# Kernel optimization log

Measured on AMD Instinct MI355X. Metric: run time of the kernel, lower is better.

The kernel has to match this reference:

```python
import jax, jax.numpy as jnp
import numpy as np

N_LAYERS = 5
HID = 64
N_FF = 512
N_VOCAB = 500
N_NODES = 50000
N_EDGES = 800000


def setup_inputs() -> dict:
    key = jax.random.key(0)
    ks = jax.random.split(key, 12)
    x = jax.random.randint(ks[0], (N_NODES,), 0, N_VOCAB)
    edge_index = jax.random.randint(ks[1], (2, N_EDGES), 0, N_NODES)
    edge_attr = jax.random.normal(ks[2], (N_EDGES, 4), dtype=jnp.float32)
    s = 1.0 / float(np.sqrt(HID))
    vert_emb = jax.random.normal(ks[3], (N_VOCAB + 1, HID), dtype=jnp.float32) * s
    vert_emb = vert_emb.at[N_VOCAB].set(0.0)  # padding_idx row
    edge_emb_w = jax.random.normal(ks[4], (4, HID), dtype=jnp.float32) * 0.5
    edge_lin_w = jax.random.normal(ks[5], (N_LAYERS, HID, HID), dtype=jnp.float32) * s
    rel_w = jax.random.normal(ks[6], (N_LAYERS, HID, HID), dtype=jnp.float32) * s
    rel_b = jnp.zeros((N_LAYERS, HID), dtype=jnp.float32)
    root_w = jax.random.normal(ks[7], (N_LAYERS, HID, HID), dtype=jnp.float32) * s
    res_w = jax.random.normal(ks[8], (N_LAYERS, HID, HID), dtype=jnp.float32) * s
    head_w1 = jax.random.normal(ks[9], (HID, N_FF), dtype=jnp.float32) * s
    head_b1 = jnp.zeros((N_FF,), dtype=jnp.float32)
    head_w2 = jax.random.normal(ks[10], (N_FF, 1), dtype=jnp.float32) * (1.0 / float(np.sqrt(N_FF)))
    head_b2 = jnp.zeros((1,), dtype=jnp.float32)
    return dict(x=x, edge_index=edge_index, edge_attr=edge_attr, vert_emb=vert_emb,
                edge_emb_w=edge_emb_w, edge_lin_w=edge_lin_w, rel_w=rel_w, rel_b=rel_b,
                root_w=root_w, res_w=res_w, head_w1=head_w1, head_b1=head_b1,
                head_w2=head_w2, head_b2=head_b2)


def reference(x, edge_index, edge_attr, vert_emb, edge_emb_w, edge_lin_w, rel_w, rel_b,
              root_w, res_w, head_w1, head_b1, head_w2, head_b2):
    src, dst = edge_index[0], edge_index[1]
    h = vert_emb[x]                         # [N, HID] embedding lookup
    ea = edge_attr @ edge_emb_w             # [E, HID] edge embedding
    n = h.shape[0]
    for l in range(N_LAYERS):
        ea_l = ea @ edge_lin_w[l]           # ResGraphModule.edge_lin
        # GraphConv(aggr='add'): lin_rel(scatter_add(x_src * e)) + lin_root(x)
        msg = h[src] * ea_l                 # [E, HID] gather + modulate
        agg = jax.ops.segment_sum(msg, dst, num_segments=n)
        out = agg @ rel_w[l] + rel_b[l] + h @ root_w[l]
        out = jax.nn.relu(out)
        h = out + h @ res_w[l]              # residual branch (res_lin)
    # head MLP (dropout is identity in eval mode); torch GELU is exact erf GELU
    hft = jax.nn.gelu(h @ head_w1 + head_b1, approximate=False)
    return hft @ head_w2 + head_b2          # [N, 1]
```

## Files before the change

kernel.cpp:

```cpp
#include <hip/hip_runtime.h>
#include <math.h>

#define HID 64
#define NLAY 5
#define NFF 512

typedef __attribute__((ext_vector_type(8))) short bf16x8;
typedef __attribute__((ext_vector_type(4))) float f32x4;

__device__ __forceinline__ unsigned short f2bf(float x) {
  unsigned int b = __float_as_uint(x);
  b += 0x7FFFu + ((b >> 16) & 1u);
  return (unsigned short)(b >> 16);
}
__device__ __forceinline__ float bf2f(unsigned short u) {
  return __uint_as_float((unsigned int)u << 16);
}

__global__ void prep_all_kernel(const float* __restrict__ edge_emb_w,
                                const float* __restrict__ edge_lin_w,
                                const float* __restrict__ w1,
                                const float* __restrict__ rel_w,
                                const float* __restrict__ root_w,
                                const float* __restrict__ res_w,
                                float* __restrict__ Wl,
                                unsigned short* __restrict__ w1bhi,
                                unsigned short* __restrict__ w1blo,
                                unsigned short* __restrict__ nwhi,
                                unsigned short* __restrict__ nwlo) {
  int bid = blockIdx.x;
  int tid = threadIdx.x;
  if (bid < 5) {
    int j = tid >> 6;
    int d = tid & 63;
    const float* ew = edge_emb_w + j * HID;
    const float* lw = edge_lin_w + bid * HID * HID;
    float acc = 0.f;
#pragma unroll
    for (int k = 0; k < HID; ++k) acc = fmaf(ew[k], lw[k * HID + d], acc);
    Wl[(bid * 4 + j) * HID + d] = acc;
  } else if (bid < 21) {
    int t = (bid - 5) * 256 + tid;
    int f = t >> 6;
    int l = t & 63;
    int kt = f >> 5;
    int nt = f & 31;
    int krow = kt * 32 + (l >> 4) * 8;
    int col = nt * 16 + (l & 15);
#pragma unroll
    for (int j = 0; j < 8; ++j) {
      float v = w1[(size_t)(krow + j) * NFF + col];
      unsigned short hi = f2bf(v);
      unsigned short lo = f2bf(v - bf2f(hi));
      w1bhi[(size_t)t * 8 + j] = hi;
      w1blo[(size_t)t * 8 + j] = lo;
    }
  } else {
    int mi = bid - 21;
    int layer = mi / 3, mat = mi % 3;
    const float* W = (mat == 0 ? rel_w : (mat == 1 ? root_w : res_w)) +
                     (size_t)layer * HID * HID;
#pragma unroll
    for (int half = 0; half < 2; ++half) {
      int t = half * 256 + tid;
      int f = t >> 6, l = t & 63;
      int kt = f >> 2, nt = f & 3;
      int krow = kt * 32 + (l >> 4) * 8;
      int col = nt * 16 + (l & 15);
#pragma unroll
      for (int j = 0; j < 8; ++j) {
        float v = W[(size_t)(krow + j) * HID + col];
        unsigned short hi = f2bf(v);
        unsigned short lo = f2bf(v - bf2f(hi));
        size_t off = (((size_t)mi * 8 + f) * 64 + l) * 8 + j;
        nwhi[off] = hi;
        nwlo[off] = lo;
      }
    }
  }
}

__global__ void embed_kernel(const int* __restrict__ x,
                             const float* __restrict__ vert_emb,
                             float* __restrict__ h,
                             unsigned short* __restrict__ h16,
                             int* __restrict__ deg, int n) {
  int idx = blockIdx.x * blockDim.x + threadIdx.x;
  if (idx >= n * HID) return;
  int node = idx >> 6;
  int d = idx & 63;
  float v = vert_emb[x[node] * HID + d];
  h[idx] = v;
  h16[idx] = f2bf(v);
  if (d == 0) deg[node] = 0;
}


__global__ void hist_kernel(const int* __restrict__ dst, int* __restrict__ deg, int E) {
  int e = blockIdx.x * blockDim.x + threadIdx.x;
  if (e < E) atomicAdd(&deg[dst[e]], 1);
}

__global__ void bsum_kernel(const int* __restrict__ deg, int* __restrict__ bsum, int n) {
  __shared__ int s[256];
  int t = threadIdx.x;
  int i = blockIdx.x * 256 + t;
  s[t] = (i < n) ? deg[i] : 0;
  __syncthreads();
#pragma unroll
  for (int off = 128; off > 0; off >>= 1) {
    if (t < off) s[t] += s[t + off];
    __syncthreads();
  }
  if (t == 0) bsum[blockIdx.x] = s[0];
}

__global__ void bscan_kernel(const int* __restrict__ bsum, int* __restrict__ boff, int nb) {
  __shared__ int s[256];
  int t = threadIdx.x;
  int v = (t < nb) ? bsum[t] : 0;
  s[t] = v;
  __syncthreads();
#pragma unroll
  for (int off = 1; off < 256; off <<= 1) {
    int u = (t >= off) ? s[t - off] : 0;
    __syncthreads();
    s[t] += u;
    __syncthreads();
  }
  if (t < nb) boff[t] = s[t] - v;
}

__global__ void scan3_kernel(const int* __restrict__ deg, const int* __restrict__ boff,
                             int* __restrict__ row_ptr, int* __restrict__ cursor, int n) {
  __shared__ int s[256];
  int t = threadIdx.x;
  int i = blockIdx.x * 256 + t;
  int v = (i < n) ? deg[i] : 0;
  s[t] = v;
  __syncthreads();
#pragma unroll
  for (int off = 1; off < 256; off <<= 1) {
    int u = (t >= off) ? s[t - off] : 0;
    __syncthreads();
    s[t] += u;
    __syncthreads();
  }
  if (i < n) {
    int excl = boff[blockIdx.x] + s[t] - v;
    row_ptr[i] = excl;
    cursor[i] = excl;
    if (i == n - 1) row_ptr[n] = excl + v;
  }
}

__global__ void scatter_kernel(const int* __restrict__ src,
                               const int* __restrict__ dst,
                               const float4* __restrict__ edge_attr,
                               int* __restrict__ cursor,
                               float4* __restrict__ csr2, int E) {
  int e = blockIdx.x * blockDim.x + threadIdx.x;
  if (e >= E) return;
  int pos = atomicAdd(&cursor[dst[e]], 1);
  csr2[(size_t)2 * pos] = edge_attr[e];
  float4 m;
  m.x = __int_as_float(src[e]);
  m.y = 0.f; m.z = 0.f; m.w = 0.f;
  csr2[(size_t)2 * pos + 1] = m;
}

__global__ __launch_bounds__(256, 4)
void layer_fused_kernel(const int* __restrict__ row_ptr,
                        const float4* __restrict__ csr2,
                        const float* __restrict__ Wl,
                        const float* __restrict__ h,
                        const unsigned short* __restrict__ h16,
                        const unsigned short* __restrict__ nwhi,
                        const unsigned short* __restrict__ nwlo,
                        const float* __restrict__ rel_b,
                        float* __restrict__ hn,
                        unsigned short* __restrict__ hn16, int n) {
  __shared__ float sagg[16][65];
  int tid = threadIdx.x;
  int w = tid >> 6;
  int d = tid & 63;
  int base = blockIdx.x * 16;
  float w0 = Wl[d], w1_ = Wl[HID + d], w2_ = Wl[2 * HID + d], w3_ = Wl[3 * HID + d];
  const int* csri = (const int*)csr2;
  for (int i = 0; i < 4; ++i) {
    int node = base + w * 4 + i;
    float P0 = 0.f, P1 = 0.f, P2 = 0.f, P3 = 0.f;
    if (node < n) {
      int beg = __builtin_amdgcn_readfirstlane(row_ptr[node]);
      int end = __builtin_amdgcn_readfirstlane(row_ptr[node + 1]);
      int j = beg;
      for (; j + 16 <= end; j += 16) {
        int ss[16];
        float hh[16];
        float4 ee[16];
#pragma unroll
        for (int u = 0; u < 16; ++u) ss[u] = csri[((size_t)2 * (j + u) + 1) * 4];
#pragma unroll
        for (int u = 0; u < 16; ++u) hh[u] = bf2f(h16[(size_t)ss[u] * HID + d]);
#pragma unroll
        for (int u = 0; u < 16; ++u) ee[u] = csr2[(size_t)2 * (j + u)];
#pragma unroll
        for (int u = 0; u < 16; ++u) {
          P0 = fmaf(ee[u].x, hh[u], P0);
          P1 = fmaf(ee[u].y, hh[u], P1);
          P2 = fmaf(ee[u].z, hh[u], P2);
          P3 = fmaf(ee[u].w, hh[u], P3);
        }
      }
      for (; j + 4 <= end; j += 4) {
        int ss[4];
        float hh[4];
        float4 ee[4];
#pragma unroll
        for (int u = 0; u < 4; ++u) ss[u] = csri[((size_t)2 * (j + u) + 1) * 4];
#pragma unroll
        for (int u = 0; u < 4; ++u) hh[u] = bf2f(h16[(size_t)ss[u] * HID + d]);
#pragma unroll
        for (int u = 0; u < 4; ++u) ee[u] = csr2[(size_t)2 * (j + u)];
#pragma unroll
        for (int u = 0; u < 4; ++u) {
          P0 = fmaf(ee[u].x, hh[u], P0);
          P1 = fmaf(ee[u].y, hh[u], P1);
          P2 = fmaf(ee[u].z, hh[u], P2);
          P3 = fmaf(ee[u].w, hh[u], P3);
        }
      }
      for (; j < end; ++j) {
        int s0 = csri[((size_t)2 * j + 1) * 4];
        float4 e0 = csr2[(size_t)2 * j];
        float h0 = bf2f(h16[(size_t)s0 * HID + d]);
        P0 = fmaf(e0.x, h0, P0);
        P1 = fmaf(e0.y, h0, P1);
        P2 = fmaf(e0.z, h0, P2);
        P3 = fmaf(e0.w, h0, P3);
      }
    }
    float acc = fmaf(P3, w3_, fmaf(P2, w2_, fmaf(P1, w1_, P0 * w0)));
    sagg[w * 4 + i][d] = acc;
  }
  __syncthreads();
  int l = tid & 63;
  int q = l & 15;
  int g = l >> 4;
  int node = base + q;
  if (node >= n) node = n - 1;
  bf16x8 aghi[2], aglo[2], ahhi[2], ahlo[2];
#pragma unroll
  for (int kt = 0; kt < 2; ++kt) {
    int koff = kt * 32 + g * 8;
    const float* hp = h + (size_t)node * HID + koff;
    ahhi[kt] = *(const bf16x8*)(h16 + (size_t)node * HID + koff);
#pragma unroll
    for (int j = 0; j < 8; ++j) {
      float av = sagg[q][koff + j];
      unsigned short hi = f2bf(av);
      aghi[kt][j] = (short)hi;
      aglo[kt][j] = (short)f2bf(av - bf2f(hi));
      float r = hp[j] - bf2f((unsigned short)ahhi[kt][j]);
      ahlo[kt][j] = (short)f2bf(r);
    }
  }
  f32x4 aR = {0.f, 0.f, 0.f, 0.f};
  f32x4 aO = {0.f, 0.f, 0.f, 0.f};
  f32x4 aS = {0.f, 0.f, 0.f, 0.f};
#pragma unroll
  for (int kt = 0; kt < 2; ++kt) {
    int f = kt * 4 + w;
    const bf16x8* bRh = (const bf16x8*)(nwhi + (((size_t)0 * 8 + f) * 64 + l) * 8);
    const bf16x8* bRl = (const bf16x8*)(nwlo + (((size_t)0 * 8 + f) * 64 + l) * 8);
    const bf16x8* bOh = (const bf16x8*)(nwhi + (((size_t)1 * 8 + f) * 64 + l) * 8);
    const bf16x8* bOl = (const bf16x8*)(nwlo + (((size_t)1 * 8 + f) * 64 + l) * 8);
    const bf16x8* bSh = (const bf16x8*)(nwhi + (((size_t)2 * 8 + f) * 64 + l) * 8);
    const bf16x8* bSl = (const bf16x8*)(nwlo + (((size_t)2 * 8 + f) * 64 + l) * 8);
    aR = __builtin_amdgcn_mfma_f32_16x16x32_bf16(aglo[kt], *bRh, aR, 0, 0, 0);
    aR = __builtin_amdgcn_mfma_f32_16x16x32_bf16(aghi[kt], *bRl, aR, 0, 0, 0);
    aR = __builtin_amdgcn_mfma_f32_16x16x32_bf16(aghi[kt], *bRh, aR, 0, 0, 0);
    aO = __builtin_amdgcn_mfma_f32_16x16x32_bf16(ahlo[kt], *bOh, aO, 0, 0, 0);
    aO = __builtin_amdgcn_mfma_f32_16x16x32_bf16(ahhi[kt], *bOl, aO, 0, 0, 0);
    aO = __builtin_amdgcn_mfma_f32_16x16x32_bf16(ahhi[kt], *bOh, aO, 0, 0, 0);
    aS = __builtin_amdgcn_mfma_f32_16x16x32_bf16(ahlo[kt], *bSh, aS, 0, 0, 0);
    aS = __builtin_amdgcn_mfma_f32_16x16x32_bf16(ahhi[kt], *bSl, aS, 0, 0, 0);
    aS = __builtin_amdgcn_mfma_f32_16x16x32_bf16(ahhi[kt], *bSh, aS, 0, 0, 0);
  }
  int col = w * 16 + q;
  float bd = rel_b[col];
#pragma unroll
  for (int r = 0; r < 4; ++r) {
    int nd = base + g * 4 + r;
    if (nd < n) {
      float v = fmaxf(aR[r] + aO[r] + bd, 0.f) + aS[r];
      hn[(size_t)nd * HID + col] = v;
      hn16[(size_t)nd * HID + col] = f2bf(v);
    }
  }
}

__global__ __launch_bounds__(256, 4)
void head_kernel(const float* __restrict__ h,
                 const unsigned short* __restrict__ h16,
                 const unsigned short* __restrict__ w1bhi,
                 const unsigned short* __restrict__ w1blo,
                 const float* __restrict__ b1,
                 const float* __restrict__ w2,
                 const float* __restrict__ b2,
                 float* __restrict__ out, int n) {
  __shared__ float red[4][16];
  int tid = threadIdx.x;
  int w = tid >> 6;
  int l = tid & 63;
  int row = l & 15;
  int g = l >> 4;
  int base = blockIdx.x * 16;
  int node = base + row;
  if (node >= n) node = n - 1;
  f32x4 acc[8];
#pragma unroll
  for (int t = 0; t < 8; ++t) acc[t] = (f32x4){0.f, 0.f, 0.f, 0.f};
#pragma unroll
  for (int kt = 0; kt < 2; ++kt) {
    int koff = kt * 32 + g * 8;
    bf16x8 ahi = *(const bf16x8*)(h16 + (size_t)node * HID + koff);
    const float* hp = h + (size_t)node * HID + koff;
    bf16x8 alo;
#pragma unroll
    for (int j = 0; j < 8; ++j) {
      float r = hp[j] - bf2f((unsigned short)ahi[j]);
      alo[j] = (short)f2bf(r);
    }
#pragma unroll
    for (int t = 0; t < 8; ++t) {
      int f = kt * 32 + w * 8 + t;
      bf16x8 bhi = *(const bf16x8*)(w1bhi + (size_t)f * 512 + l * 8);
      bf16x8 blo = *(const bf16x8*)(w1blo + (size_t)f * 512 + l * 8);
      acc[t] = __builtin_amdgcn_mfma_f32_16x16x32_bf16(alo, bhi, acc[t], 0, 0, 0);
      acc[t] = __builtin_amdgcn_mfma_f32_16x16x32_bf16(ahi, blo, acc[t], 0, 0, 0);
      acc[t] = __builtin_amdgcn_mfma_f32_16x16x32_bf16(ahi, bhi, acc[t], 0, 0, 0);
    }
  }
  float s0 = 0.f, s1 = 0.f, s2 = 0.f, s3 = 0.f;
#pragma unroll
  for (int t = 0; t < 8; ++t) {
    int ff = (w * 8 + t) * 16 + row;
    float bb = b1[ff];
    float ww = w2[ff];
    float xv, gl;
    xv = acc[t][0] + bb; gl = 0.5f * xv * (1.f + erff(xv * 0.70710678118654752f)); s0 = fmaf(gl, ww, s0);
    xv = acc[t][1] + bb; gl = 0.5f * xv * (1.f + erff(xv * 0.70710678118654752f)); s1 = fmaf(gl, ww, s1);
    xv = acc[t][2] + bb; gl = 0.5f * xv * (1.f + erff(xv * 0.70710678118654752f)); s2 = fmaf(gl, ww, s2);
    xv = acc[t][3] + bb; gl = 0.5f * xv * (1.f + erff(xv * 0.70710678118654752f)); s3 = fmaf(gl, ww, s3);
  }
#pragma unroll
  for (int off = 1; off < 16; off <<= 1) {
    s0 += __shfl_xor(s0, off);
    s1 += __shfl_xor(s1, off);
    s2 += __shfl_xor(s2, off);
    s3 += __shfl_xor(s3, off);
  }
  if ((l & 15) == 0) {
    red[w][g * 4 + 0] = s0;
    red[w][g * 4 + 1] = s1;
    red[w][g * 4 + 2] = s2;
    red[w][g * 4 + 3] = s3;
  }
  __syncthreads();
  if (tid < 16 && base + tid < n)
    out[base + tid] = red[0][tid] + red[1][tid] + red[2][tid] + red[3][tid] + b2[0];
}

extern "C" void kernel_launch(void* const* d_in, const int* in_sizes, int n_in,
                              void* d_out, int out_size, void* d_ws, size_t ws_size,
                              hipStream_t stream) {
  const int*   x          = (const int*)d_in[0];
  const int*   edge_index = (const int*)d_in[1];
  const float* edge_attr  = (const float*)d_in[2];
  const float* vert_emb   = (const float*)d_in[3];
  const float* edge_emb_w = (const float*)d_in[4];
  const float* edge_lin_w = (const float*)d_in[5];
  const float* rel_w      = (const float*)d_in[6];
  const float* rel_b      = (const float*)d_in[7];
  const float* root_w     = (const float*)d_in[8];
  const float* res_w      = (const float*)d_in[9];
  const float* w1         = (const float*)d_in[10];
  const float* b1         = (const float*)d_in[11];
  const float* w2         = (const float*)d_in[12];
  const float* b2         = (const float*)d_in[13];

  const int n = in_sizes[0];
  const int E = in_sizes[2] / 4;
  const int* src = edge_index;
  const int* dst = edge_index + E;
  const int nb = (n + 255) / 256;

  float* ws   = (float*)d_ws;
  float* Wl   = ws;
  float* hA   = ws + 2048;
  float* hB   = hA + (size_t)n * HID;
  float4* csr2 = (float4*)(hB + (size_t)n * HID);
  int* row_ptr = (int*)(csr2 + (size_t)2 * E);
  int* cursor  = row_ptr + (n + 1);
  int* deg     = cursor + n;
  int* bsum    = deg + n;
  int* boff    = bsum + 256;
  unsigned short* w1bhi = (unsigned short*)(((size_t)(boff + 256) + 15) & ~(size_t)15);
  unsigned short* w1blo = w1bhi + 64 * 512;
  unsigned short* nwhi  = w1blo + 64 * 512;
  unsigned short* nwlo  = nwhi + NLAY * 3 * 4096;
  unsigned short* h16A  = nwlo + NLAY * 3 * 4096;
  unsigned short* h16B  = h16A + (size_t)n * HID;

  prep_all_kernel<<<dim3(36), dim3(256), 0, stream>>>(
      edge_emb_w, edge_lin_w, w1, rel_w, root_w, res_w,
      Wl, w1bhi, w1blo, nwhi, nwlo);

  int totalHD = n * HID;
  embed_kernel<<<dim3((totalHD + 255) / 256), dim3(256), 0, stream>>>(
      x, vert_emb, hA, h16A, deg, n);

  hist_kernel<<<dim3((E + 255) / 256), dim3(256), 0, stream>>>(dst, deg, E);
  bsum_kernel<<<dim3(nb), dim3(256), 0, stream>>>(deg, bsum, n);
  bscan_kernel<<<dim3(1), dim3(256), 0, stream>>>(bsum, boff, nb);
  scan3_kernel<<<dim3(nb), dim3(256), 0, stream>>>(deg, boff, row_ptr, cursor, n);
  scatter_kernel<<<dim3((E + 255) / 256), dim3(256), 0, stream>>>(
      src, dst, (const float4*)edge_attr, cursor, csr2, E);

  float* hc = hA;
  float* hx = hB;
  unsigned short* h16c = h16A;
  unsigned short* h16x = h16B;
  for (int l = 0; l < NLAY; ++l) {
    layer_fused_kernel<<<dim3((n + 15) / 16), dim3(256), 0, stream>>>(
        row_ptr, csr2, Wl + l * 4 * HID, hc, h16c,
        nwhi + (size_t)l * 3 * 4096, nwlo + (size_t)l * 3 * 4096,
        rel_b + l * HID, hx, h16x, n);
    float* t = hc; hc = hx; hx = t;
    unsigned short* t16 = h16c; h16c = h16x; h16x = t16;
  }

  head_kernel<<<dim3((n + 15) / 16), dim3(256), 0, stream>>>(
      hc, h16c, w1bhi, w1blo, b1, w2, b2, (float*)d_out, n);
}
```

Measured before the change: 451.3 us.

## Split layer into gather and MFMA kernels with lane-broadcast src and double-buffered loads

Each fused layer kernel is split into a gather kernel, with one wave per node, and a separate MFMA node-transform kernel that reads the aggregate from a global buffer. The gather loads up to 64 source indices with one coalesced load per wave and broadcasts them with readlane. It then double-buffers chunks of 8 edge loads so the next chunk is in flight while the current one is accumulated. This aims to raise memory-level parallelism and reduce per-edge index load latency. In exchange it adds a global round trip for the aggregate (n×64 floats written and read per layer) and a second kernel launch per layer.

```diff
diff --git a/kernel.cpp b/kernel.cpp
--- a/kernel.cpp
+++ b/kernel.cpp
@@ -169,95 +169,102 @@
   csr2[(size_t)2 * pos + 1] = m;
 }
 
+#define GLOAD_CHUNK(HH, EE, c)                                            \
+  {                                                                       \
+    int cbase = 8 * (c);                                                  \
+    _Pragma("unroll")                                                     \
+    for (int u = 0; u < 8; ++u) {                                         \
+      int idx = cbase + u;                                                \
+      int cl = (idx < bcnt) ? idx : 0;                                    \
+      int su = __builtin_amdgcn_readlane(srcv, cl);                       \
+      HH[u] = bf2f(h16[(size_t)su * HID + d]);                            \
+      float4 ev = csr2[(size_t)2 * (blk + cl)];                           \
+      if (idx >= bcnt) { ev.x = 0.f; ev.y = 0.f; ev.z = 0.f; ev.w = 0.f; } \
+      EE[u] = ev;                                                         \
+    }                                                                     \
+  }
+
+#define GCONSUME_CHUNK(HH, EE)                                            \
+  {                                                                       \
+    _Pragma("unroll")                                                     \
+    for (int u = 0; u < 8; ++u) {                                         \
+      P0 = fmaf(EE[u].x, HH[u], P0);                                      \
+      P1 = fmaf(EE[u].y, HH[u], P1);                                      \
+      P2 = fmaf(EE[u].z, HH[u], P2);                                      \
+      P3 = fmaf(EE[u].w, HH[u], P3);                                      \
+    }                                                                     \
+  }
+
 __global__ __launch_bounds__(256, 4)
-void layer_fused_kernel(const int* __restrict__ row_ptr,
-                        const float4* __restrict__ csr2,
-                        const float* __restrict__ Wl,
-                        const float* __restrict__ h,
-                        const unsigned short* __restrict__ h16,
-                        const unsigned short* __restrict__ nwhi,
-                        const unsigned short* __restrict__ nwlo,
-                        const float* __restrict__ rel_b,
-                        float* __restrict__ hn,
-                        unsigned short* __restrict__ hn16, int n) {
-  __shared__ float sagg[16][65];
+void gather_kernel(const int* __restrict__ row_ptr,
+                   const float4* __restrict__ csr2,
+                   const float* __restrict__ Wl,
+                   const unsigned short* __restrict__ h16,
+                   float* __restrict__ agg, int n) {
+  int wid = threadIdx.x >> 6;
+  int d = threadIdx.x & 63;
+  int node = blockIdx.x * 4 + wid;
+  if (node >= n) return;
+  int beg = __builtin_amdgcn_readfirstlane(row_ptr[node]);
+  int end = __builtin_amdgcn_readfirstlane(row_ptr[node + 1]);
+  const int* csri = (const int*)csr2;
+  float P0 = 0.f, P1 = 0.f, P2 = 0.f, P3 = 0.f;
+  for (int blk = beg; blk < end; blk += 64) {
+    int bcnt = end - blk;
+    if (bcnt > 64) bcnt = 64;
+    int li = (d < bcnt) ? d : bcnt - 1;
+    int srcv = csri[((size_t)2 * (blk + li) + 1) * 4];
+    int nch = (bcnt + 7) >> 3;
+    float hhA[8], hhB[8];
+    float4 eeA[8], eeB[8];
+    GLOAD_CHUNK(hhA, eeA, 0)
+    int c = 0;
+    while (c < nch) {
+      if (c + 1 < nch) {
+        GLOAD_CHUNK(hhB, eeB, c + 1)
+        GCONSUME_CHUNK(hhA, eeA)
+        ++c;
+        if (c + 1 < nch) { GLOAD_CHUNK(hhA, eeA, c + 1) }
+        GCONSUME_CHUNK(hhB, eeB)
+        ++c;
+      } else {
+        GCONSUME_CHUNK(hhA, eeA)
+        ++c;
+      }
+    }
+  }
+  float w0 = Wl[d], w1_ = Wl[HID + d], w2_ = Wl[2 * HID + d], w3_ = Wl[3 * HID + d];
+  float acc = fmaf(P3, w3_, fmaf(P2, w2_, fmaf(P1, w1_, P0 * w0)));
+  agg[(size_t)node * HID + d] = acc;
+}
+
+__global__ __launch_bounds__(256, 4)
+void node_mfma_kernel(const float* __restrict__ h,
+                      const unsigned short* __restrict__ h16,
+                      const float* __restrict__ agg,
+                      const unsigned short* __restrict__ nwhi,
+                      const unsigned short* __restrict__ nwlo,
+                      const float* __restrict__ rel_b,
+                      float* __restrict__ hn,
+                      unsigned short* __restrict__ hn16, int n) {
   int tid = threadIdx.x;
   int w = tid >> 6;
-  int d = tid & 63;
-  int base = blockIdx.x * 16;
-  float w0 = Wl[d], w1_ = Wl[HID + d], w2_ = Wl[2 * HID + d], w3_ = Wl[3 * HID + d];
-  const int* csri = (const int*)csr2;
-  for (int i = 0; i < 4; ++i) {
-    int node = base + w * 4 + i;
-    float P0 = 0.f, P1 = 0.f, P2 = 0.f, P3 = 0.f;
-    if (node < n) {
-      int beg = __builtin_amdgcn_readfirstlane(row_ptr[node]);
-      int end = __builtin_amdgcn_readfirstlane(row_ptr[node + 1]);
-      int j = beg;
-      for (; j + 16 <= end; j += 16) {
-        int ss[16];
-        float hh[16];
-        float4 ee[16];
-#pragma unroll
-        for (int u = 0; u < 16; ++u) ss[u] = csri[((size_t)2 * (j + u) + 1) * 4];
-#pragma unroll
-        for (int u = 0; u < 16; ++u) hh[u] = bf2f(h16[(size_t)ss[u] * HID + d]);
-#pragma unroll
-        for (int u = 0; u < 16; ++u) ee[u] = csr2[(size_t)2 * (j + u)];
-#pragma unroll
-        for (int u = 0; u < 16; ++u) {
-          P0 = fmaf(ee[u].x, hh[u], P0);
-          P1 = fmaf(ee[u].y, hh[u], P1);
-          P2 = fmaf(ee[u].z, hh[u], P2);
-          P3 = fmaf(ee[u].w, hh[u], P3);
-        }
-      }
-      for (; j + 4 <= end; j += 4) {
-        int ss[4];
-        float hh[4];
-        float4 ee[4];
-#pragma unroll
-        for (int u = 0; u < 4; ++u) ss[u] = csri[((size_t)2 * (j + u) + 1) * 4];
-#pragma unroll
-        for (int u = 0; u < 4; ++u) hh[u] = bf2f(h16[(size_t)ss[u] * HID + d]);
-#pragma unroll
-        for (int u = 0; u < 4; ++u) ee[u] = csr2[(size_t)2 * (j + u)];
-#pragma unroll
-        for (int u = 0; u < 4; ++u) {
-          P0 = fmaf(ee[u].x, hh[u], P0);
-          P1 = fmaf(ee[u].y, hh[u], P1);
-          P2 = fmaf(ee[u].z, hh[u], P2);
-          P3 = fmaf(ee[u].w, hh[u], P3);
-        }
-      }
-      for (; j < end; ++j) {
-        int s0 = csri[((size_t)2 * j + 1) * 4];
-        float4 e0 = csr2[(size_t)2 * j];
-        float h0 = bf2f(h16[(size_t)s0 * HID + d]);
-        P0 = fmaf(e0.x, h0, P0);
-        P1 = fmaf(e0.y, h0, P1);
-        P2 = fmaf(e0.z, h0, P2);
-        P3 = fmaf(e0.w, h0, P3);
-      }
-    }
-    float acc = fmaf(P3, w3_, fmaf(P2, w2_, fmaf(P1, w1_, P0 * w0)));
-    sagg[w * 4 + i][d] = acc;
-  }
-  __syncthreads();
   int l = tid & 63;
   int q = l & 15;
   int g = l >> 4;
+  int base = blockIdx.x * 16;
   int node = base + q;
   if (node >= n) node = n - 1;
   bf16x8 aghi[2], aglo[2], ahhi[2], ahlo[2];
 #pragma unroll
   for (int kt = 0; kt < 2; ++kt) {
     int koff = kt * 32 + g * 8;
+    const float* ap = agg + (size_t)node * HID + koff;
     const float* hp = h + (size_t)node * HID + koff;
     ahhi[kt] = *(const bf16x8*)(h16 + (size_t)node * HID + koff);
 #pragma unroll
     for (int j = 0; j < 8; ++j) {
-      float av = sagg[q][koff + j];
+      float av = ap[j];
       unsigned short hi = f2bf(av);
       aghi[kt][j] = (short)hi;
       aglo[kt][j] = (short)f2bf(av - bf2f(hi));
@@ -400,7 +407,8 @@
   float* Wl   = ws;
   float* hA   = ws + 2048;
   float* hB   = hA + (size_t)n * HID;
-  float4* csr2 = (float4*)(hB + (size_t)n * HID);
+  float* agg  = hB + (size_t)n * HID;
+  float4* csr2 = (float4*)(agg + (size_t)n * HID);
   int* row_ptr = (int*)(csr2 + (size_t)2 * E);
   int* cursor  = row_ptr + (n + 1);
   int* deg     = cursor + n;
@@ -433,9 +441,10 @@
   unsigned short* h16c = h16A;
   unsigned short* h16x = h16B;
   for (int l = 0; l < NLAY; ++l) {
-    layer_fused_kernel<<<dim3((n + 15) / 16), dim3(256), 0, stream>>>(
-        row_ptr, csr2, Wl + l * 4 * HID, hc, h16c,
-        nwhi + (size_t)l * 3 * 4096, nwlo + (size_t)l * 3 * 4096,
+    gather_kernel<<<dim3((n + 3) / 4), dim3(256), 0, stream>>>(
+        row_ptr, csr2, Wl + l * 4 * HID, h16c, agg, n);
+    node_mfma_kernel<<<dim3((n + 15) / 16), dim3(256), 0, stream>>>(
+        hc, h16c, agg, nwhi + (size_t)l * 3 * 4096, nwlo + (size_t)l * 3 * 4096,
         rel_b + l * HID, hx, h16x, n);
     float* t = hc; hc = hx; hx = t;
     unsigned short* t16 = h16c; h16c = h16x; h16x = t16;
```

New measurement: 513.9 us. +13.9%, slower.
